# Performance work log

Measured on AMD Instinct MI355X. Metric: run time of the kernel, lower is better.

## Reference

```python
import jax, jax.numpy as jnp
import numpy as np

B, D, K, U = 4096, 1024, 5, 1024  # batch, input_dim, num_basis, units


def setup_inputs() -> dict:
    key = jax.random.key(0)
    k1, k2, k3 = jax.random.split(key, 3)
    x = jax.random.normal(k1, (B, D), dtype=jnp.float32)
    basis_weights = jax.random.normal(k2, (D, K, U), dtype=jnp.float32) * 0.02
    bias = jax.random.normal(k3, (U,), dtype=jnp.float32) * 0.02
    return {"x": x, "basis_weights": basis_weights, "bias": bias}


def reference(x, basis_weights, bias):
    # Polynomial basis expansion: x^0, x^1, ..., x^{K-1}  -> (B, D, K)
    num_basis = basis_weights.shape[1]
    powers = jnp.arange(num_basis, dtype=x.dtype)
    basis = x[..., None] ** powers  # x**0 == 1, matching tf.ones_like branch
    # Fused: einsum('bik,ikj->bij') followed by reduce_sum over i == 'bik,ikj->bj'.
    # Avoids materializing the (B, D, U) intermediate of the original.
    out = jnp.einsum("bik,ikj->bj", basis, basis_weights) + bias
    # tf.nn.gelu defaults to exact (non-approximate) GELU.
    return jax.nn.gelu(out, approximate=False)
```

## Files before the change

kernel.cpp:

```cpp
#include <hip/hip_runtime.h>
#include <hip/hip_bf16.h>
#include <math.h>


#define B_DIM 4096
#define D_DIM 1024
#define U_DIM 1024
#define KT2 4096
#define NKB 128

typedef unsigned short ushort_t;
typedef __attribute__((ext_vector_type(8))) short bf16x8;
typedef __attribute__((ext_vector_type(4))) float f32x4;

__device__ __forceinline__ ushort_t f2bf(float f) {
  union { float f; unsigned int u; } v;
  v.f = f;
  unsigned int r = v.u + 0x7FFFu + ((v.u >> 16) & 1u);
  return (ushort_t)(r >> 16);
}

__device__ __forceinline__ void load_lds16(const ushort_t* g, ushort_t* l) {
  __builtin_amdgcn_global_load_lds(
      (const __attribute__((address_space(1))) ushort_t*)g,
      (__attribute__((address_space(3))) ushort_t*)l, 16, 0, 0);
}

__device__ __forceinline__ float gelu_exact(float v) {
  return 0.5f * v * (1.0f + erff(v * 0.70710678118654752f));
}

__device__ __forceinline__ unsigned int fbits(float f) {
  union { float f; unsigned int u; } v; v.f = f; return v.u;
}

__device__ __forceinline__ bf16x8 build_afrag(float xa, float xb) {
  const float a2 = xa * xa, b2 = xb * xb;
  const float a3 = a2 * xa, a4 = a2 * a2;
  const float b3 = b2 * xb, b4 = b2 * b2;
  union { bf16x8 v; unsigned int d[4]; } r;
  r.d[0] = __builtin_amdgcn_perm(fbits(a2), fbits(xa), 0x07060302u);
  r.d[1] = __builtin_amdgcn_perm(fbits(a4), fbits(a3), 0x07060302u);
  r.d[2] = __builtin_amdgcn_perm(fbits(b2), fbits(xb), 0x07060302u);
  r.d[3] = __builtin_amdgcn_perm(fbits(b4), fbits(b3), 0x07060302u);
  return r.v;
}


__global__ __launch_bounds__(256) void w_pack_fold_kernel(
    const float* __restrict__ W, ushort_t* __restrict__ Bp, float* __restrict__ part) {
  const int t    = threadIdx.x;
  const int wave = t >> 6;
  const int lane = t & 63;
  const int bx   = blockIdx.x;
  const int n16  = blockIdx.y;
  {
    const int kblk = bx * 4 + wave;
    const int jj   = lane & 15;
    const int ko   = lane >> 4;
    const int j    = n16 * 16 + jj;
    const int i0   = kblk * 8 + ko * 2;
    ushort_t o[8];
#pragma unroll
    for (int t2 = 0; t2 < 2; ++t2) {
      const int i = i0 + t2;
#pragma unroll
      for (int e = 0; e < 4; ++e) {
        const int r = i * 5 + e + 1;
        o[t2 * 4 + e] = f2bf(W[(size_t)r * U_DIM + j]);
      }
    }
    *(uint4*)(Bp + ((size_t)n16 * NKB + kblk) * 512 + lane * 8) = *(const uint4*)o;
  }
  __shared__ float red[16][17];
  {
    const int jj = t & 15;
    const int ii = t >> 4;
    const int i1 = bx * 32 + ii;
    const int i2 = i1 + 16;
    const int j  = n16 * 16 + jj;
    red[ii][jj] = W[(size_t)(i1 * 5) * U_DIM + j] + W[(size_t)(i2 * 5) * U_DIM + j];
  }
  __syncthreads();
  if (t < 16) {
    float s = 0.0f;
#pragma unroll
    for (int ii = 0; ii < 16; ++ii) s += red[ii][t];
    part[(size_t)bx * U_DIM + n16 * 16 + t] = s;
  }
}

__global__ __launch_bounds__(256, 2) void gemm_kernel(
    const float* __restrict__ x, const ushort_t* __restrict__ Bp,
    const float* __restrict__ bias, const float* __restrict__ part,
    float* __restrict__ C) {
  __shared__ ushort_t lds[2][16 * 512];

  const int tid  = threadIdx.x;
  const int wave = tid >> 6;
  const int lane = tid & 63;
  const int wm   = wave >> 1;
  const int wn   = wave & 1;
  const int tileN = blockIdx.x * 128;
  const int tileM = blockIdx.y * 64;

  const ushort_t* gsrc[4];
  int ldst[4];
#pragma unroll
  for (int s = 0; s < 4; ++s) {
    const int u    = wave * 4 + s;
    const int nloc = u & 7;
    const int kloc = u >> 3;
    gsrc[s] = Bp + ((size_t)((tileN >> 4) + nloc) * NKB + kloc) * 512 + lane * 8;
    ldst[s] = u * 512 + lane * 8;
  }

  const float* xptr[2];
#pragma unroll
  for (int mf = 0; mf < 2; ++mf)
    xptr[mf] = x + (size_t)(tileM + wm * 32 + mf * 16 + (lane & 15)) * D_DIM
                 + (lane >> 4) * 2;

  f32x4 acc[2][4];
  const f32x4 zero = {0.0f, 0.0f, 0.0f, 0.0f};
#pragma unroll
  for (int mf = 0; mf < 2; ++mf)
#pragma unroll
    for (int nf = 0; nf < 4; ++nf) acc[mf][nf] = zero;

#define STAGE(bb, it)                                                   \
  do {                                                                  \
    _Pragma("unroll")                                                   \
    for (int s = 0; s < 4; ++s)                                         \
      load_lds16(gsrc[s] + (size_t)(it) * 1024, &lds[bb][ldst[s]]);     \
  } while (0)

  float2 xc[2][2], xn[2][2];
#pragma unroll
  for (int kl = 0; kl < 2; ++kl)
#pragma unroll
    for (int mf = 0; mf < 2; ++mf)
      xc[kl][mf] = *(const float2*)(xptr[mf] + (size_t)kl * 8);

  STAGE(0, 0);
  __syncthreads();

  for (int it = 0; it < 64; ++it) {
    const int cur = it & 1;
    if (it + 1 < 64) {
      STAGE(cur ^ 1, it + 1);
#pragma unroll
      for (int kl = 0; kl < 2; ++kl)
#pragma unroll
        for (int mf = 0; mf < 2; ++mf)
          xn[kl][mf] = *(const float2*)(xptr[mf] + ((size_t)(it + 1) * 2 + kl) * 8);
    }

#pragma unroll
    for (int kl = 0; kl < 2; ++kl) {
      bf16x8 a[2], b[4];
#pragma unroll
      for (int mf = 0; mf < 2; ++mf)
        a[mf] = build_afrag(xc[kl][mf].x, xc[kl][mf].y);
#pragma unroll
      for (int nf = 0; nf < 4; ++nf)
        b[nf] = *(const bf16x8*)&lds[cur][(kl * 8 + wn * 4 + nf) * 512 + lane * 8];
#pragma unroll
      for (int mf = 0; mf < 2; ++mf)
#pragma unroll
        for (int nf = 0; nf < 4; ++nf)
          acc[mf][nf] = __builtin_amdgcn_mfma_f32_16x16x32_bf16(a[mf], b[nf], acc[mf][nf], 0, 0, 0);
    }

#pragma unroll
    for (int kl = 0; kl < 2; ++kl)
#pragma unroll
      for (int mf = 0; mf < 2; ++mf)
        xc[kl][mf] = xn[kl][mf];

    __syncthreads();
  }
#undef STAGE

  const int crow0 = tileM + wm * 32 + (lane >> 4) * 4;
  const int ccol0 = tileN + wn * 64 + (lane & 15);
#pragma unroll
  for (int nf = 0; nf < 4; ++nf) {
    const int col = ccol0 + nf * 16;
    float bv = bias[col];
#pragma unroll 8
    for (int g = 0; g < 32; ++g) bv += part[(size_t)g * U_DIM + col];
#pragma unroll
    for (int mf = 0; mf < 2; ++mf) {
#pragma unroll
      for (int r = 0; r < 4; ++r) {
        const int row = crow0 + mf * 16 + r;
        C[(size_t)row * U_DIM + col] = gelu_exact(acc[mf][nf][r] + bv);
      }
    }
  }
}

__global__ void fallback_kernel(const float* __restrict__ x, const float* __restrict__ W,
                                const float* __restrict__ bias, float* __restrict__ out) {
  int j  = blockIdx.x * 256 + threadIdx.x;
  int b0 = blockIdx.y * 16;
  float acc[16];
#pragma unroll
  for (int t = 0; t < 16; ++t) acc[t] = 0.0f;
  for (int i = 0; i < D_DIM; ++i) {
    const float* wr = W + (size_t)i * 5 * U_DIM + j;
    float w0 = wr[0 * U_DIM], w1 = wr[1 * U_DIM], w2 = wr[2 * U_DIM];
    float w3 = wr[3 * U_DIM], w4 = wr[4 * U_DIM];
#pragma unroll
    for (int t = 0; t < 16; ++t) {
      float xv = x[(size_t)(b0 + t) * D_DIM + i];
      float x2 = xv * xv;
      acc[t] += w0 + xv * w1 + x2 * w2 + x2 * xv * w3 + x2 * x2 * w4;
    }
  }
  float bv = bias[j];
#pragma unroll
  for (int t = 0; t < 16; ++t)
    out[(size_t)(b0 + t) * U_DIM + j] = gelu_exact(acc[t] + bv);
}

extern "C" void kernel_launch(void* const* d_in, const int* in_sizes, int n_in,
                              void* d_out, int out_size, void* d_ws, size_t ws_size,
                              hipStream_t stream) {
  const float* x    = (const float*)d_in[0];
  const float* W    = (const float*)d_in[1];
  const float* bias = (const float*)d_in[2];
  float* out = (float*)d_out;

  const size_t szB = (size_t)U_DIM * KT2 * sizeof(ushort_t);
  const size_t szP = (size_t)32 * U_DIM * sizeof(float);

  if (ws_size >= szB + szP) {
    ushort_t* Bp   = (ushort_t*)d_ws;
    float*    part = (float*)((char*)d_ws + szB);
    w_pack_fold_kernel<<<dim3(32, U_DIM / 16), 256, 0, stream>>>(W, Bp, part);
    gemm_kernel<<<dim3(U_DIM / 128, B_DIM / 64), 256, 0, stream>>>(x, Bp, bias, part, out);
  } else {
    fallback_kernel<<<dim3(U_DIM / 256, B_DIM / 16), 256, 0, stream>>>(x, W, bias, out);
  }
}
```

Measured before the change: 162.9 us.

## Shrink GEMM N-tile to 64, deepen x prefetch, coarsen weight pack blocks

```diff
diff --git a/kernel.cpp b/kernel.cpp
--- a/kernel.cpp
+++ b/kernel.cpp
@@ -54,8 +54,9 @@
   const int lane = t & 63;
   const int bx   = blockIdx.x;
   const int n16  = blockIdx.y;
-  {
-    const int kblk = bx * 4 + wave;
+#pragma unroll
+  for (int s = 0; s < 4; ++s) {
+    const int kblk = bx * 16 + wave * 4 + s;
     const int jj   = lane & 15;
     const int ko   = lane >> 4;
     const int j    = n16 * 16 + jj;
@@ -76,10 +77,14 @@
   {
     const int jj = t & 15;
     const int ii = t >> 4;
-    const int i1 = bx * 32 + ii;
-    const int i2 = i1 + 16;
     const int j  = n16 * 16 + jj;
-    red[ii][jj] = W[(size_t)(i1 * 5) * U_DIM + j] + W[(size_t)(i2 * 5) * U_DIM + j];
+    float s = 0.0f;
+#pragma unroll
+    for (int g = 0; g < 8; ++g) {
+      const int i = bx * 128 + ii + g * 16;
+      s += W[(size_t)(i * 5) * U_DIM + j];
+    }
+    red[ii][jj] = s;
   }
   __syncthreads();
   if (t < 16) {
@@ -90,29 +95,26 @@
   }
 }
 
-__global__ __launch_bounds__(256, 2) void gemm_kernel(
+__global__ __launch_bounds__(256, 4) void gemm_kernel(
     const float* __restrict__ x, const ushort_t* __restrict__ Bp,
     const float* __restrict__ bias, const float* __restrict__ part,
     float* __restrict__ C) {
-  __shared__ ushort_t lds[2][16 * 512];
+  __shared__ ushort_t lds[2][8 * 512];
 
   const int tid  = threadIdx.x;
   const int wave = tid >> 6;
   const int lane = tid & 63;
   const int wm   = wave >> 1;
   const int wn   = wave & 1;
-  const int tileN = blockIdx.x * 128;
+  const int tileN = blockIdx.x * 64;
   const int tileM = blockIdx.y * 64;
 
-  const ushort_t* gsrc[4];
-  int ldst[4];
-#pragma unroll
-  for (int s = 0; s < 4; ++s) {
-    const int u    = wave * 4 + s;
-    const int nloc = u & 7;
-    const int kloc = u >> 3;
-    gsrc[s] = Bp + ((size_t)((tileN >> 4) + nloc) * NKB + kloc) * 512 + lane * 8;
-    ldst[s] = u * 512 + lane * 8;
+  const ushort_t* gsrc[2];
+  int ldst[2];
+#pragma unroll
+  for (int s = 0; s < 2; ++s) {
+    gsrc[s] = Bp + ((size_t)((tileN >> 4) + wave) * NKB + s) * 512 + lane * 8;
+    ldst[s] = (s * 4 + wave) * 512 + lane * 8;
   }
 
   const float* xptr[2];
@@ -121,75 +123,79 @@
     xptr[mf] = x + (size_t)(tileM + wm * 32 + mf * 16 + (lane & 15)) * D_DIM
                  + (lane >> 4) * 2;
 
-  f32x4 acc[2][4];
+  f32x4 acc[2][2];
   const f32x4 zero = {0.0f, 0.0f, 0.0f, 0.0f};
 #pragma unroll
   for (int mf = 0; mf < 2; ++mf)
 #pragma unroll
-    for (int nf = 0; nf < 4; ++nf) acc[mf][nf] = zero;
+    for (int nf = 0; nf < 2; ++nf) acc[mf][nf] = zero;
 
 #define STAGE(bb, it)                                                   \
   do {                                                                  \
     _Pragma("unroll")                                                   \
-    for (int s = 0; s < 4; ++s)                                         \
+    for (int s = 0; s < 2; ++s)                                         \
       load_lds16(gsrc[s] + (size_t)(it) * 1024, &lds[bb][ldst[s]]);     \
   } while (0)
 
-  float2 xc[2][2], xn[2][2];
+  float2 xc[2][2], xn1[2][2], xn2[2][2];
 #pragma unroll
   for (int kl = 0; kl < 2; ++kl)
 #pragma unroll
-    for (int mf = 0; mf < 2; ++mf)
-      xc[kl][mf] = *(const float2*)(xptr[mf] + (size_t)kl * 8);
+    for (int mf = 0; mf < 2; ++mf) {
+      xc[kl][mf]  = *(const float2*)(xptr[mf] + kl * 8);
+      xn1[kl][mf] = *(const float2*)(xptr[mf] + 16 + kl * 8);
+    }
 
   STAGE(0, 0);
   __syncthreads();
 
   for (int it = 0; it < 64; ++it) {
     const int cur = it & 1;
-    if (it + 1 < 64) {
-      STAGE(cur ^ 1, it + 1);
+    if (it + 1 < 64) STAGE(cur ^ 1, it + 1);
+    if (it + 2 < 64) {
 #pragma unroll
       for (int kl = 0; kl < 2; ++kl)
 #pragma unroll
         for (int mf = 0; mf < 2; ++mf)
-          xn[kl][mf] = *(const float2*)(xptr[mf] + ((size_t)(it + 1) * 2 + kl) * 8);
+          xn2[kl][mf] = *(const float2*)(xptr[mf] + (size_t)(it + 2) * 16 + kl * 8);
     }
 
 #pragma unroll
     for (int kl = 0; kl < 2; ++kl) {
-      bf16x8 a[2], b[4];
+      bf16x8 a[2], b[2];
 #pragma unroll
       for (int mf = 0; mf < 2; ++mf)
         a[mf] = build_afrag(xc[kl][mf].x, xc[kl][mf].y);
 #pragma unroll
-      for (int nf = 0; nf < 4; ++nf)
-        b[nf] = *(const bf16x8*)&lds[cur][(kl * 8 + wn * 4 + nf) * 512 + lane * 8];
+      for (int nf = 0; nf < 2; ++nf)
+        b[nf] = *(const bf16x8*)&lds[cur][(kl * 4 + wn * 2 + nf) * 512 + lane * 8];
 #pragma unroll
       for (int mf = 0; mf < 2; ++mf)
 #pragma unroll
-        for (int nf = 0; nf < 4; ++nf)
+        for (int nf = 0; nf < 2; ++nf)
           acc[mf][nf] = __builtin_amdgcn_mfma_f32_16x16x32_bf16(a[mf], b[nf], acc[mf][nf], 0, 0, 0);
     }
 
 #pragma unroll
     for (int kl = 0; kl < 2; ++kl)
 #pragma unroll
-      for (int mf = 0; mf < 2; ++mf)
-        xc[kl][mf] = xn[kl][mf];
+      for (int mf = 0; mf < 2; ++mf) {
+        xc[kl][mf]  = xn1[kl][mf];
+        xn1[kl][mf] = xn2[kl][mf];
+      }
 
     __syncthreads();
   }
 #undef STAGE
 
   const int crow0 = tileM + wm * 32 + (lane >> 4) * 4;
-  const int ccol0 = tileN + wn * 64 + (lane & 15);
-#pragma unroll
-  for (int nf = 0; nf < 4; ++nf) {
+  const int ccol0 = tileN + wn * 32 + (lane & 15);
+#pragma unroll
+  for (int nf = 0; nf < 2; ++nf) {
     const int col = ccol0 + nf * 16;
     float bv = bias[col];
-#pragma unroll 8
-    for (int g = 0; g < 32; ++g) bv += part[(size_t)g * U_DIM + col];
+#pragma unroll
+    for (int g = 0; g < 8; ++g) bv += part[(size_t)g * U_DIM + col];
 #pragma unroll
     for (int mf = 0; mf < 2; ++mf) {
 #pragma unroll
@@ -234,13 +240,13 @@
   float* out = (float*)d_out;
 
   const size_t szB = (size_t)U_DIM * KT2 * sizeof(ushort_t);
-  const size_t szP = (size_t)32 * U_DIM * sizeof(float);
+  const size_t szP = (size_t)8 * U_DIM * sizeof(float);
 
   if (ws_size >= szB + szP) {
     ushort_t* Bp   = (ushort_t*)d_ws;
     float*    part = (float*)((char*)d_ws + szB);
-    w_pack_fold_kernel<<<dim3(32, U_DIM / 16), 256, 0, stream>>>(W, Bp, part);
-    gemm_kernel<<<dim3(U_DIM / 128, B_DIM / 64), 256, 0, stream>>>(x, Bp, bias, part, out);
+    w_pack_fold_kernel<<<dim3(8, U_DIM / 16), 256, 0, stream>>>(W, Bp, part);
+    gemm_kernel<<<dim3(U_DIM / 64, B_DIM / 64), 256, 0, stream>>>(x, Bp, bias, part, out);
   } else {
     fallback_kernel<<<dim3(U_DIM / 256, B_DIM / 16), 256, 0, stream>>>(x, W, bias, out);
   }
```

After: 219.7 us. 1.35x slower.
